# Kernel tuning notes

Measured on AMD Instinct MI355X. Metric: run time of the kernel, lower is better.

## Reference

```python
import jax, jax.numpy as jnp
import numpy as np

BLOCK = 8  # block_size from init_kwargs


def _zigzag(n):
    # Same traversal as zigzag_indices() in the original module.
    idx = np.zeros(n * n, dtype=np.int64)
    i = j = 0
    for k in range(n * n):
        idx[k] = i * n + j
        if (i + j) % 2 == 0:  # moving up-right
            if j == n - 1:
                i += 1
            elif i == 0:
                j += 1
            else:
                i -= 1
                j += 1
        else:  # moving down-left
            if i == n - 1:
                j += 1
            elif j == 0:
                i += 1
            else:
                i += 1
                j -= 1
    return idx


def _dct_basis(N):
    # dct() with norm=None is DCT-II: V[k] = 2 * sum_n x[n] cos(pi*(2n+1)k/(2N))
    k = np.arange(N)[:, None].astype(np.float64)
    nn = np.arange(N)[None, :].astype(np.float64)
    return (2.0 * np.cos(np.pi * (2.0 * nn + 1.0) * k / (2.0 * N))).astype(np.float32)


def setup_inputs() -> dict:
    key = jax.random.key(0)
    img = jax.random.normal(key, (16, 3, 512, 512), dtype=jnp.float32)
    return {"img": img}


def reference(img):
    B = BLOCK
    bs, c, h, w = img.shape
    hb, wb = h // B, w // B
    n = hb * wb
    m = hb  # square grid: m = sqrt(n)

    # split_blocks: unfold(2,B,B).unfold(3,B,B) -> [bs,c,hb,wb,B,B] -> [bs,n,c,B,B]
    blocks = (
        img.reshape(bs, c, hb, B, wb, B)
        .transpose(0, 2, 4, 1, 3, 5)
        .reshape(bs, n, c, B, B)
    )

    # dct_2d with norm=None as separable matmuls against the DCT-II basis
    C = jnp.asarray(_dct_basis(B))  # [B, B] basis, C[k, x]
    z = jnp.einsum("uh,vw,bnchw->bncuv", C, C, blocks)  # [bs,n,c,B,B]

    # frequencyFeat: zigzag-reorder the B*B coeffs, then tile blocks into an m x m map
    zz = jnp.asarray(_zigzag(B))
    flat = z.reshape(bs, n, c, B * B)[..., zz]  # [bs,n,c,B*B]
    feat = (
        flat.reshape(bs, m, m, c, B * B)
        .transpose(0, 3, 4, 1, 2)
        .reshape(bs, c * B * B, m, m)
    )
    return feat
```

## Files before the change

### kernel.cpp

```cpp
#include <hip/hip_runtime.h>


typedef float f32x4 __attribute__((ext_vector_type(4)));

#define K1 1.9615705608064609f
#define K2 1.8477590650225735f
#define K3 1.6629392246050905f
#define K4 1.4142135623730951f
#define K5 1.1111404660392044f
#define K6 0.7653668647301796f
#define K7 0.3901806440322565f

#define DCT8(x0,x1,x2,x3,x4,x5,x6,x7, y0,y1,y2,y3,y4,y5,y6,y7) do {        \
    float s0=(x0)+(x7), s1=(x1)+(x6), s2=(x2)+(x5), s3=(x3)+(x4);          \
    float d0=(x0)-(x7), d1=(x1)-(x6), d2=(x2)-(x5), d3=(x3)-(x4);          \
    float e0=s0+s3, e1=s1+s2, o0=s0-s3, o1=s1-s2;                          \
    y0 = 2.0f*(e0+e1);                                                     \
    y4 = K4*(e0-e1);                                                       \
    y2 = K2*o0 + K6*o1;                                                    \
    y6 = K6*o0 - K2*o1;                                                    \
    y1 = K1*d0 + K3*d1 + K5*d2 + K7*d3;                                    \
    y3 = K3*d0 - K7*d1 - K1*d2 - K5*d3;                                    \
    y5 = K5*d0 - K1*d1 + K7*d2 + K3*d3;                                    \
    y7 = K7*d0 - K5*d1 + K3*d2 - K1*d3;                                    \
} while (0)

#define LOADROW(r)                                                          \
    const float4 L##r##a = *reinterpret_cast<const float4*>(src + (r)*512); \
    const float4 L##r##b = *reinterpret_cast<const float4*>(src + (r)*512 + 4);

#define ROWDCT(r)                                                          \
    DCT8(L##r##a.x,L##r##a.y,L##r##a.z,L##r##a.w,                          \
         L##r##b.x,L##r##b.y,L##r##b.z,L##r##b.w,                          \
         t##r##0,t##r##1,t##r##2,t##r##3,t##r##4,t##r##5,t##r##6,t##r##7);

#define COLPHASE(v, PACK) do {                                             \
    float z0,z1,z2,z3,z4,z5,z6,z7;                                         \
    DCT8(t0##v,t1##v,t2##v,t3##v,t4##v,t5##v,t6##v,t7##v,                  \
         z0,z1,z2,z3,z4,z5,z6,z7);                                         \
    float* buf = lds + (((v)&1) << 11);                                    \
    float* w = buf + wr;                                                   \
    w[0]=z0; w[256]=z1; w[512]=z2; w[768]=z3;                              \
    w[1024]=z4; w[1280]=z5; w[1536]=z6; w[1792]=z7;                        \
    asm volatile("s_waitcnt lgkmcnt(0)" ::: "memory");                     \
    __builtin_amdgcn_s_barrier();                                          \
    const f32x4 r0 = *reinterpret_cast<const f32x4*>(buf + (tid << 2));    \
    const f32x4 r1 = *reinterpret_cast<const f32x4*>(buf + 1024 + (tid << 2)); \
    const int p0 = (int)(((PACK) >> (bil*8)) & 63);                        \
    const int p1 = (int)(((PACK) >> (bil*8 + 32)) & 63);                   \
    __builtin_nontemporal_store(r0,                                        \
        reinterpret_cast<f32x4*>(dst + (size_t)p0*4096));                  \
    __builtin_nontemporal_store(r1,                                        \
        reinterpret_cast<f32x4*>(dst + (size_t)p1*4096));                  \
} while (0)

__global__ __launch_bounds__(256) void dct2d_zigzag_kernel(
    const float* __restrict__ img, float* __restrict__ out)
{
    __shared__ float lds[4096];

    const int tid = threadIdx.x;
    const int wg  = blockIdx.x;
    const int bc  = wg >> 4;
    const int big = wg & 15;
    const int bj  = tid & 63;
    const int bil = tid >> 6;

    const float* __restrict__ src =
        img + (size_t)bc * 262144 + (size_t)(big*4 + bil) * 4096 + (size_t)bj * 8;

    float* __restrict__ dst =
        out + (size_t)bc * 262144 + (size_t)big * 256 + (size_t)bj * 4;

    const int wr = bil*64 + bj;

    LOADROW(0) LOADROW(1) LOADROW(2) LOADROW(3)
    LOADROW(4) LOADROW(5) LOADROW(6) LOADROW(7)

    float t00,t01,t02,t03,t04,t05,t06,t07;
    float t10,t11,t12,t13,t14,t15,t16,t17;
    float t20,t21,t22,t23,t24,t25,t26,t27;
    float t30,t31,t32,t33,t34,t35,t36,t37;
    float t40,t41,t42,t43,t44,t45,t46,t47;
    float t50,t51,t52,t53,t54,t55,t56,t57;
    float t60,t61,t62,t63,t64,t65,t66,t67;
    float t70,t71,t72,t73,t74,t75,t76,t77;

    ROWDCT(0) ROWDCT(1) ROWDCT(2) ROWDCT(3)
    ROWDCT(4) ROWDCT(5) ROWDCT(6) ROWDCT(7)

    COLPHASE(0, 0x2315140A09030200ULL);
    COLPHASE(1, 0x242216130B080401ULL);
    COLPHASE(2, 0x30252117120C0705ULL);
    COLPHASE(3, 0x312F262018110D06ULL);
    COLPHASE(4, 0x39322E271F19100EULL);
    COLPHASE(5, 0x3A38332D281E1A0FULL);
    COLPHASE(6, 0x3E3B37342C291D1BULL);
    COLPHASE(7, 0x3F3D3C36352B2A1CULL);
}

extern "C" void kernel_launch(void* const* d_in, const int* in_sizes, int n_in,
                              void* d_out, int out_size, void* d_ws, size_t ws_size,
                              hipStream_t stream)
{
    const float* img = (const float*)d_in[0];
    float* out = (float*)d_out;
    dct2d_zigzag_kernel<<<768, 256, 0, stream>>>(img, out);
}
```

Baseline: 97.53 us.

## Split each 8x8 block across two lanes and use shuffles instead of LDS

```diff
diff --git a/kernel.cpp b/kernel.cpp
--- a/kernel.cpp
+++ b/kernel.cpp
@@ -1,7 +1,5 @@
 #include <hip/hip_runtime.h>
 
-
-typedef float f32x4 __attribute__((ext_vector_type(4)));
 
 #define K1 1.9615705608064609f
 #define K2 1.8477590650225735f
@@ -34,69 +32,65 @@
          L##r##b.x,L##r##b.y,L##r##b.z,L##r##b.w,                          \
          t##r##0,t##r##1,t##r##2,t##r##3,t##r##4,t##r##5,t##r##6,t##r##7);
 
-#define COLPHASE(v, PACK) do {                                             \
-    float z0,z1,z2,z3,z4,z5,z6,z7;                                         \
-    DCT8(t0##v,t1##v,t2##v,t3##v,t4##v,t5##v,t6##v,t7##v,                  \
-         z0,z1,z2,z3,z4,z5,z6,z7);                                         \
-    float* buf = lds + (((v)&1) << 11);                                    \
-    float* w = buf + wr;                                                   \
-    w[0]=z0; w[256]=z1; w[512]=z2; w[768]=z3;                              \
-    w[1024]=z4; w[1280]=z5; w[1536]=z6; w[1792]=z7;                        \
-    asm volatile("s_waitcnt lgkmcnt(0)" ::: "memory");                     \
-    __builtin_amdgcn_s_barrier();                                          \
-    const f32x4 r0 = *reinterpret_cast<const f32x4*>(buf + (tid << 2));    \
-    const f32x4 r1 = *reinterpret_cast<const f32x4*>(buf + 1024 + (tid << 2)); \
-    const int p0 = (int)(((PACK) >> (bil*8)) & 63);                        \
-    const int p1 = (int)(((PACK) >> (bil*8 + 32)) & 63);                   \
-    __builtin_nontemporal_store(r0,                                        \
-        reinterpret_cast<f32x4*>(dst + (size_t)p0*4096));                  \
-    __builtin_nontemporal_store(r1,                                        \
-        reinterpret_cast<f32x4*>(dst + (size_t)p1*4096));                  \
+#define COLP(c, pa0,pa1,pa2,pa3, pb0,pb1,pb2,pb3) do {                     \
+    const float o0f = __shfl_xor(t0##c, 32);                               \
+    const float o1f = __shfl_xor(t1##c, 32);                               \
+    const float o2f = __shfl_xor(t2##c, 32);                               \
+    const float o3f = __shfl_xor(t3##c, 32);                               \
+    if (lane < 32) {                                                       \
+        float s0 = t0##c + o3f, s1 = t1##c + o2f;                          \
+        float s2 = t2##c + o1f, s3 = t3##c + o0f;                          \
+        float e0 = s0+s3, e1 = s1+s2, q0 = s0-s3, q1 = s1-s2;              \
+        __builtin_nontemporal_store(2.0f*(e0+e1), dst + (size_t)(pa0)*4096); \
+        __builtin_nontemporal_store(K2*q0+K6*q1,  dst + (size_t)(pa1)*4096); \
+        __builtin_nontemporal_store(K4*(e0-e1),   dst + (size_t)(pa2)*4096); \
+        __builtin_nontemporal_store(K6*q0-K2*q1,  dst + (size_t)(pa3)*4096); \
+    } else {                                                               \
+        float d0 = o0f - t3##c, d1 = o1f - t2##c;                          \
+        float d2 = o2f - t1##c, d3 = o3f - t0##c;                          \
+        __builtin_nontemporal_store(K1*d0+K3*d1+K5*d2+K7*d3, dst + (size_t)(pb0)*4096); \
+        __builtin_nontemporal_store(K3*d0-K7*d1-K1*d2-K5*d3, dst + (size_t)(pb1)*4096); \
+        __builtin_nontemporal_store(K5*d0-K1*d1+K7*d2+K3*d3, dst + (size_t)(pb2)*4096); \
+        __builtin_nontemporal_store(K7*d0-K5*d1+K3*d2-K1*d3, dst + (size_t)(pb3)*4096); \
+    }                                                                      \
 } while (0)
 
 __global__ __launch_bounds__(256) void dct2d_zigzag_kernel(
     const float* __restrict__ img, float* __restrict__ out)
 {
-    __shared__ float lds[4096];
-
-    const int tid = threadIdx.x;
-    const int wg  = blockIdx.x;
-    const int bc  = wg >> 4;
-    const int big = wg & 15;
-    const int bj  = tid & 63;
-    const int bil = tid >> 6;
+    const int gid  = blockIdx.x * 256 + threadIdx.x;
+    const int lane = gid & 63;
+    const int wid  = gid >> 6;
+    const int hr   = wid & 1;
+    const int bi   = (wid >> 1) & 63;
+    const int bc   = wid >> 7;
+    const int part = lane >> 5;
+    const int bj   = hr * 32 + (lane & 31);
 
     const float* __restrict__ src =
-        img + (size_t)bc * 262144 + (size_t)(big*4 + bil) * 4096 + (size_t)bj * 8;
+        img + (size_t)bc * 262144 + (size_t)bi * 4096
+            + (size_t)part * 2048 + (size_t)bj * 8;
 
     float* __restrict__ dst =
-        out + (size_t)bc * 262144 + (size_t)big * 256 + (size_t)bj * 4;
-
-    const int wr = bil*64 + bj;
+        out + (size_t)bc * 262144 + (size_t)bi * 64 + bj;
 
     LOADROW(0) LOADROW(1) LOADROW(2) LOADROW(3)
-    LOADROW(4) LOADROW(5) LOADROW(6) LOADROW(7)
 
     float t00,t01,t02,t03,t04,t05,t06,t07;
     float t10,t11,t12,t13,t14,t15,t16,t17;
     float t20,t21,t22,t23,t24,t25,t26,t27;
     float t30,t31,t32,t33,t34,t35,t36,t37;
-    float t40,t41,t42,t43,t44,t45,t46,t47;
-    float t50,t51,t52,t53,t54,t55,t56,t57;
-    float t60,t61,t62,t63,t64,t65,t66,t67;
-    float t70,t71,t72,t73,t74,t75,t76,t77;
 
     ROWDCT(0) ROWDCT(1) ROWDCT(2) ROWDCT(3)
-    ROWDCT(4) ROWDCT(5) ROWDCT(6) ROWDCT(7)
 
-    COLPHASE(0, 0x2315140A09030200ULL);
-    COLPHASE(1, 0x242216130B080401ULL);
-    COLPHASE(2, 0x30252117120C0705ULL);
-    COLPHASE(3, 0x312F262018110D06ULL);
-    COLPHASE(4, 0x39322E271F19100EULL);
-    COLPHASE(5, 0x3A38332D281E1A0FULL);
-    COLPHASE(6, 0x3E3B37342C291D1BULL);
-    COLPHASE(7, 0x3F3D3C36352B2A1CULL);
+    COLP(0,  0,  3, 10, 21,   2,  9, 20, 35);
+    COLP(1,  1,  8, 19, 34,   4, 11, 22, 36);
+    COLP(2,  5, 12, 23, 37,   7, 18, 33, 48);
+    COLP(3,  6, 17, 32, 47,  13, 24, 38, 49);
+    COLP(4, 14, 25, 39, 50,  16, 31, 46, 57);
+    COLP(5, 15, 30, 45, 56,  26, 40, 51, 58);
+    COLP(6, 27, 41, 52, 59,  29, 44, 55, 62);
+    COLP(7, 28, 43, 54, 61,  42, 53, 60, 63);
 }
 
 extern "C" void kernel_launch(void* const* d_in, const int* in_sizes, int n_in,
@@ -105,5 +99,5 @@
 {
     const float* img = (const float*)d_in[0];
     float* out = (float*)d_out;
-    dct2d_zigzag_kernel<<<768, 256, 0, stream>>>(img, out);
+    dct2d_zigzag_kernel<<<1536, 256, 0, stream>>>(img, out);
 }
```

Result: no change. 98.23 us (+0.7%).
